# Kernel tuning notes

Hardware: AMD Instinct MI355X
Metric: run time of the kernel (lower is better)

The kernel has to match this reference:

```python
import jax, jax.numpy as jnp
import numpy as np

B, S, D = 4, 2048, 1024
E, ES, K = 16, 256, 4  # n_experts, expert_size, top-k (= n_heads)
STD_GATE = 0.02


def setup_inputs() -> dict:
    key = jax.random.key(0)
    k1, k2, k3, k4 = jax.random.split(key, 4)
    x = jax.random.normal(k1, (B, S, D), dtype=jnp.float32)
    # init per module: gate ~ N(0, d^-0.5), keys ~ N(0, d^-0.5), values ~ N(0, size^-0.5)
    w_gate = jax.random.normal(k2, (E, D), dtype=jnp.float32) * (D ** -0.5)
    keys = jax.random.normal(k3, (E, D, ES), dtype=jnp.float32) * (D ** -0.5)
    values = jax.random.normal(k4, (E, ES, D), dtype=jnp.float32) * ((E * ES) ** -0.5)
    return {"x": x, "w_gate": w_gate, "keys": keys, "values": values}


def reference(x, w_gate, keys, values):
    # sigma-MoE forward (selection_mode='sigmoid', activation=relu,
    # num_selected = n_heads = K, no bias, no dropout, eval mode)
    xt = x.reshape(-1, D)                         # [T, D]
    T = xt.shape[0]
    logits = xt @ w_gate.T                        # [T, E]
    sel = jax.nn.sigmoid(logits)                  # sigmoid gating
    sel_val, sel_idx = jax.lax.top_k(sel, K)      # [T, K]
    # sparse gate weights as dense [T, E] mask (zeros for unselected experts)
    gate_w = jnp.zeros((T, E), dtype=x.dtype).at[
        jnp.arange(T)[:, None], sel_idx
    ].set(sel_val)
    # per-expert hidden: h[t,e,s] = relu(sum_d x[t,d] keys[e,d,s])
    h = jax.nn.relu(jnp.einsum('td,eds->tes', xt, keys))  # [T, E, ES]
    # weighted scatter back through values: out = sum_e gate * h_e @ values_e
    out = jnp.einsum('tes,te,esv->tv', h, gate_w, values)  # [T, D]
    return out.reshape(B, S, D)
```

## Files before the change

kernel.cpp:

```cpp
#include <hip/hip_runtime.h>
#include <hip/hip_bf16.h>
#include <stdint.h>

#define T_TOK 8192
#define DIM   1024
#define NEXP  16
#define ESZ   256
#define TOPK  4
#define BM    64
#define BK    64
#define NPAIR (T_TOK*TOPK)
#define NGB   (T_TOK/32)
#define NBLK  128
#define GPB   (NGB/NBLK)
#define MAXROWS (NPAIR + NEXP*BM)
#define MAXTILES (NPAIR/BM + NEXP)

typedef __hip_bfloat16 bf16;
typedef short bf16x8 __attribute__((ext_vector_type(8)));
typedef float f32x4 __attribute__((ext_vector_type(4)));

__device__ __forceinline__ unsigned short f2bu(float f){
  __hip_bfloat16 b = __float2bfloat16(f);
  return *reinterpret_cast<unsigned short*>(&b);
}
__device__ __forceinline__ float bu2f(unsigned short u){
  __hip_bfloat16 b = *reinterpret_cast<__hip_bfloat16*>(&u);
  return __bfloat162float(b);
}

__device__ __forceinline__ void gload16(const void* g, void* l){
  __builtin_amdgcn_global_load_lds((const __attribute__((address_space(1))) void*)g,
                                   (__attribute__((address_space(3))) void*)l, 16, 0, 0);
}

__global__ __launch_bounds__(512) void k_gate(const float* __restrict__ x,
    const float* __restrict__ wg, bf16* __restrict__ xb,
    int* __restrict__ sel_idx, float* __restrict__ sel_gate,
    int* __restrict__ block_hist)
{
  __shared__ float wlds[NEXP*DIM];
  __shared__ int h[NEXP];
  const int tid = threadIdx.x;
  {
    const float4* src = (const float4*)wg;
    float4* dst = (float4*)wlds;
#pragma unroll
    for (int i=0;i<8;i++) dst[tid + i*512] = src[tid + i*512];
  }
  if (tid < NEXP) h[tid] = 0;
  __syncthreads();

  {
    const float* xs = x + (size_t)blockIdx.x*32*DIM;
    unsigned short* xd = (unsigned short*)xb + (size_t)blockIdx.x*32*DIM;
#pragma unroll
    for (int i=0;i<16;i++){
      const int f = tid + i*512;
      float4 v = *(const float4*)(xs + (size_t)f*4);
      ushort4 o; o.x=f2bu(v.x); o.y=f2bu(v.y); o.z=f2bu(v.z); o.w=f2bu(v.w);
      *(ushort4*)(xd + (size_t)f*4) = o;
    }
  }

  const int ts = tid >> 5;
  const int dc = tid & 31;
  const int t0 = blockIdx.x*32 + ts;
  const int t1 = t0 + 16;
  const float* xr0 = x + (size_t)t0*DIM;
  const float* xr1 = x + (size_t)t1*DIM;

  float acc0[NEXP], acc1[NEXP];
#pragma unroll
  for (int e=0;e<NEXP;e++){ acc0[e]=0.f; acc1[e]=0.f; }

#pragma unroll
  for (int i=0;i<8;i++){
    const int d0 = i*128 + dc*4;
    float4 xv0 = *(const float4*)(xr0 + d0);
    float4 xv1 = *(const float4*)(xr1 + d0);
#pragma unroll
    for (int e=0;e<NEXP;e++){
      float4 w = *(const float4*)(wlds + e*DIM + d0);
      acc0[e] += xv0.x*w.x + xv0.y*w.y + xv0.z*w.z + xv0.w*w.w;
      acc1[e] += xv1.x*w.x + xv1.y*w.y + xv1.z*w.z + xv1.w*w.w;
    }
  }

#pragma unroll
  for (int e=0;e<NEXP;e++){
#pragma unroll
    for (int s=1;s<32;s<<=1){
      acc0[e] += __shfl_xor(acc0[e], s);
      acc1[e] += __shfl_xor(acc1[e], s);
    }
  }

#pragma unroll
  for (int e=0;e<NEXP;e++){
    acc0[e] = 1.f/(1.f + expf(-acc0[e]));
    acc1[e] = 1.f/(1.f + expf(-acc1[e]));
  }
#pragma unroll
  for (int k=0;k<TOPK;k++){
    float b0=-2.f, b1=-2.f; int i0=0, i1=0;
#pragma unroll
    for (int e=0;e<NEXP;e++){
      if (acc0[e] > b0){ b0=acc0[e]; i0=e; }
      if (acc1[e] > b1){ b1=acc1[e]; i1=e; }
    }
    if (dc==0){
      sel_idx[t0*TOPK+k]=i0; sel_gate[t0*TOPK+k]=b0;
      sel_idx[t1*TOPK+k]=i1; sel_gate[t1*TOPK+k]=b1;
      atomicAdd(&h[i0],1); atomicAdd(&h[i1],1);
    }
    acc0[i0] = -2.f; acc1[i1] = -2.f;
  }
  __syncthreads();
  if (tid < NEXP) block_hist[blockIdx.x*NEXP + tid] = h[tid];
}

__global__ __launch_bounds__(256) void k_transpose2(const float* __restrict__ keys,
    const float* __restrict__ values, bf16* __restrict__ kT, bf16* __restrict__ vT)
{
  __shared__ float tile[32][33];
  const int which = blockIdx.y >> 4, e = blockIdx.y & 15;
  const int R = which ? ESZ : DIM, C = which ? DIM : ESZ;
  const float* src = (which ? values : keys) + (size_t)e*DIM*ESZ;
  bf16* dst = (which ? vT : kT) + (size_t)e*DIM*ESZ;
  const int ctiles = C/32;
  const int r0 = (blockIdx.x / ctiles)*32, c0 = (blockIdx.x % ctiles)*32;
  const int tx = threadIdx.x & 31, ty = threadIdx.x >> 5;
#pragma unroll
  for (int i=0;i<4;i++){ int r = ty + i*8; tile[r][tx] = src[(size_t)(r0+r)*C + c0 + tx]; }
  __syncthreads();
#pragma unroll
  for (int i=0;i<4;i++){ int r = ty + i*8; dst[(size_t)(c0+r)*R + r0 + tx] = __float2bfloat16(tile[tx][r]); }
}

__global__ void k_meta(const int* __restrict__ gh,
    int* __restrict__ tile_expert, int* __restrict__ tile_rowstart,
    int* __restrict__ tile_segend, int* __restrict__ block_base)
{
  __shared__ int sbc[NBLK][NEXP];
  __shared__ int cnt[NEXP], seg[NEXP];
  const int tid = threadIdx.x;
  for (int cell = tid; cell < NBLK*NEXP; cell += 256){
    int sb = cell >> 4, e = cell & 15;
    int s = 0;
#pragma unroll
    for (int g=0; g<GPB; ++g) s += gh[(sb*GPB+g)*NEXP + e];
    sbc[sb][e] = s;
  }
  __syncthreads();
  if (tid < NEXP){
    int s=0;
    for (int sb=0; sb<NBLK; sb++) s += sbc[sb][tid];
    cnt[tid]=s;
  }
  __syncthreads();
  if (tid==0){
    int off=0, tc=0;
    for (int e=0;e<NEXP;e++){
      seg[e]=off;
      int c = cnt[e];
      int nt = (c + BM - 1)/BM;
      for (int i=0;i<nt;i++){
        tile_expert[tc]=e; tile_rowstart[tc]=off+i*BM; tile_segend[tc]=off+c; tc++;
      }
      off += nt*BM;
    }
    for (; tc<MAXTILES; tc++) tile_expert[tc]=-1;
  }
  __syncthreads();
  if (tid < NEXP){
    int s = seg[tid];
    for (int sb=0; sb<NBLK; sb++){ block_base[sb*NEXP + tid] = s; s += sbc[sb][tid]; }
  }
}

__global__ __launch_bounds__(256) void k_scatter(const int* __restrict__ sel_idx,
    const float* __restrict__ sel_gate, const int* __restrict__ block_base,
    int* __restrict__ assign_token, float* __restrict__ assign_gate,
    int* __restrict__ inv_rows)
{
  __shared__ int wcnt[4][NEXP];
  const int p = blockIdx.x*256 + threadIdx.x;
  const int wave = threadIdx.x >> 6, lane = threadIdx.x & 63;
  const int e = sel_idx[p];
  const float g = sel_gate[p];
  int rank = 0;
#pragma unroll
  for (int ee=0; ee<NEXP; ee++){
    unsigned long long m = __ballot(e==ee);
    if (lane==0) wcnt[wave][ee] = (int)__popcll(m);
    if (e==ee) rank = (int)__popcll(m & ((1ull<<lane)-1ull));
  }
  __syncthreads();
  int pre = 0;
  for (int w=0; w<wave; w++) pre += wcnt[w][e];
  const int row = block_base[blockIdx.x*NEXP + e] + pre + rank;
  assign_token[row] = p >> 2;
  assign_gate[row]  = g;
  inv_rows[p] = row;
}

__global__ __launch_bounds__(256) void k_gemm1(
    const bf16* __restrict__ xb, const bf16* __restrict__ kT,
    const int* __restrict__ assign_token, const float* __restrict__ assign_gate,
    const int* __restrict__ tile_expert, const int* __restrict__ tile_rowstart,
    const int* __restrict__ tile_segend, bf16* __restrict__ h)
{
  __shared__ char smem[49152];
  __shared__ int   tokens_s[BM];
  __shared__ float gates_s[BM];

  const int nb = blockIdx.x, tile = blockIdx.y;
  const int e = tile_expert[tile];
  if (e < 0) return;
  const int row0 = tile_rowstart[tile];
  const int segend = tile_segend[tile];
  const int tid = threadIdx.x, wave = tid>>6, lane = tid&63;

  if (tid < BM){
    int rg = row0 + tid;
    bool vld = rg < segend;
    tokens_s[tid] = vld ? assign_token[rg] : 0;
    gates_s[tid]  = vld ? assign_gate[rg] : 0.f;
  }
  __syncthreads();

  const bf16* qA[2]; const bf16* qB[4]; int loA[2], loB[4];
#pragma unroll
  for (int i=0;i<2;i++){
    int row = i*32 + wave*8 + (lane>>3);
    int c   = (lane&7) ^ (row&7);
    qA[i] = xb + (size_t)tokens_s[row]*DIM + c*8;
    loA[i] = i*4096 + wave*1024;
  }
#pragma unroll
  for (int i=0;i<4;i++){
    int col = i*32 + wave*8 + (lane>>3);
    int c   = (lane&7) ^ (col&7);
    qB[i] = kT + ((size_t)e*ESZ + nb*128 + col)*DIM + c*8;
    loB[i] = i*4096 + wave*1024;
  }

  const int wr0 = (wave>>1)*32, wc0 = (wave&1)*64;
  int offA[2][2], offB[2][4];
#pragma unroll
  for (int kk=0;kk<2;kk++){
    int kb = kk*64 + (lane>>4)*16;
#pragma unroll
    for (int m=0;m<2;m++){ int row = wr0 + m*16 + (lane&15); offA[kk][m] = row*128 + (kb ^ ((row&7)<<4)); }
#pragma unroll
    for (int n=0;n<4;n++){ int col = wc0 + n*16 + (lane&15); offB[kk][n] = col*128 + (kb ^ ((col&7)<<4)); }
  }

  f32x4 acc[2][4];
#pragma unroll
  for (int m=0;m<2;m++)
#pragma unroll
    for (int n=0;n<4;n++) acc[m][n] = {0.f,0.f,0.f,0.f};

  auto stage = [&](int abase, int bbase){
#pragma unroll
    for (int i=0;i<2;i++){ gload16(qA[i], smem + abase + loA[i]); qA[i]+=BK; }
#pragma unroll
    for (int i=0;i<4;i++){ gload16(qB[i], smem + bbase + loB[i]); qB[i]+=BK; }
  };
  auto compute = [&](const char* Ab, const char* Bb){
#pragma unroll
    for (int kk=0;kk<2;kk++){
      bf16x8 af[2], bfr[4];
#pragma unroll
      for (int m=0;m<2;m++) af[m]  = *(const bf16x8*)(Ab + offA[kk][m]);
#pragma unroll
      for (int n=0;n<4;n++) bfr[n] = *(const bf16x8*)(Bb + offB[kk][n]);
#pragma unroll
      for (int m=0;m<2;m++)
#pragma unroll
        for (int n=0;n<4;n++)
          acc[m][n] = __builtin_amdgcn_mfma_f32_16x16x32_bf16(af[m], bfr[n], acc[m][n], 0,0,0);
    }
  };

  stage(0, 16384);
  asm volatile("s_waitcnt vmcnt(0)" ::: "memory");
  __builtin_amdgcn_s_barrier();

  for (int kt=0; kt<16; kt+=2){
    stage(8192, 32768);
    compute(smem, smem+16384);
    asm volatile("s_waitcnt vmcnt(0)" ::: "memory");
    __builtin_amdgcn_s_barrier();
    if (kt+2 < 16) stage(0, 16384);
    compute(smem+8192, smem+32768);
    asm volatile("s_waitcnt vmcnt(0)" ::: "memory");
    __builtin_amdgcn_s_barrier();
  }

#pragma unroll
  for (int m=0;m<2;m++)
#pragma unroll
    for (int n=0;n<4;n++){
      int col = wc0 + n*16 + (lane&15);
#pragma unroll
      for (int j=0;j<4;j++){
        int rloc = wr0 + m*16 + ((lane>>4)<<2) + j;
        float v = fmaxf(acc[m][n][j], 0.f) * gates_s[rloc];
        h[(size_t)(row0 + rloc)*ESZ + nb*128 + col] = __float2bfloat16(v);
      }
    }
}

__global__ __launch_bounds__(256) void k_gemm2(
    const bf16* __restrict__ h, const bf16* __restrict__ vT,
    const int* __restrict__ tile_expert, const int* __restrict__ tile_rowstart,
    bf16* __restrict__ partial)
{
  __shared__ char smem[49152];

  const int nb = blockIdx.x, tile = blockIdx.y;
  const int e = tile_expert[tile];
  if (e < 0) return;
  const int row0 = tile_rowstart[tile];
  const int tid = threadIdx.x, wave = tid>>6, lane = tid&63;

  const bf16* qA[2]; const bf16* qB[4]; int loA[2], loB[4];
#pragma unroll
  for (int i=0;i<2;i++){
    int row = i*32 + wave*8 + (lane>>3);
    int c   = (lane&7) ^ (row&7);
    qA[i] = h + (size_t)(row0 + row)*ESZ + c*8;
    loA[i] = i*4096 + wave*1024;
  }
#pragma unroll
  for (int i=0;i<4;i++){
    int col = i*32 + wave*8 + (lane>>3);
    int c   = (lane&7) ^ (col&7);
    qB[i] = vT + ((size_t)e*DIM + nb*128 + col)*ESZ + c*8;
    loB[i] = i*4096 + wave*1024;
  }

  const int wr0 = (wave>>1)*32, wc0 = (wave&1)*64;
  int offA[2][2], offB[2][4];
#pragma unroll
  for (int kk=0;kk<2;kk++){
    int kb = kk*64 + (lane>>4)*16;
#pragma unroll
    for (int m=0;m<2;m++){ int row = wr0 + m*16 + (lane&15); offA[kk][m] = row*128 + (kb ^ ((row&7)<<4)); }
#pragma unroll
    for (int n=0;n<4;n++){ int col = wc0 + n*16 + (lane&15); offB[kk][n] = col*128 + (kb ^ ((col&7)<<4)); }
  }

  f32x4 acc[2][4];
#pragma unroll
  for (int m=0;m<2;m++)
#pragma unroll
    for (int n=0;n<4;n++) acc[m][n] = {0.f,0.f,0.f,0.f};

  auto stage = [&](int abase, int bbase){
#pragma unroll
    for (int i=0;i<2;i++){ gload16(qA[i], smem + abase + loA[i]); qA[i]+=BK; }
#pragma unroll
    for (int i=0;i<4;i++){ gload16(qB[i], smem + bbase + loB[i]); qB[i]+=BK; }
  };
  auto compute = [&](const char* Ab, const char* Bb){
#pragma unroll
    for (int kk=0;kk<2;kk++){
      bf16x8 af[2], bfr[4];
#pragma unroll
      for (int m=0;m<2;m++) af[m]  = *(const bf16x8*)(Ab + offA[kk][m]);
#pragma unroll
      for (int n=0;n<4;n++) bfr[n] = *(const bf16x8*)(Bb + offB[kk][n]);
#pragma unroll
      for (int m=0;m<2;m++)
#pragma unroll
        for (int n=0;n<4;n++)
          acc[m][n] = __builtin_amdgcn_mfma_f32_16x16x32_bf16(af[m], bfr[n], acc[m][n], 0,0,0);
    }
  };

  stage(0, 16384);
  asm volatile("s_waitcnt vmcnt(0)" ::: "memory");
  __builtin_amdgcn_s_barrier();

  stage(8192, 32768);
  compute(smem, smem+16384);
  asm volatile("s_waitcnt vmcnt(0)" ::: "memory");
  __builtin_amdgcn_s_barrier();
  stage(0, 16384);
  compute(smem+8192, smem+32768);
  asm volatile("s_waitcnt vmcnt(0)" ::: "memory");
  __builtin_amdgcn_s_barrier();
  stage(8192, 32768);
  compute(smem, smem+16384);
  asm volatile("s_waitcnt vmcnt(0)" ::: "memory");
  __builtin_amdgcn_s_barrier();
  compute(smem+8192, smem+32768);

#pragma unroll
  for (int m=0;m<2;m++)
#pragma unroll
    for (int n=0;n<4;n++){
      int col = wc0 + n*16 + (lane&15);
#pragma unroll
      for (int j=0;j<4;j++){
        int rloc = wr0 + m*16 + ((lane>>4)<<2) + j;
        partial[(size_t)(row0 + rloc)*DIM + nb*128 + col] = __float2bfloat16(acc[m][n][j]);
      }
    }
}

__global__ __launch_bounds__(256) void k_reduce(const bf16* __restrict__ partial,
    const int* __restrict__ inv_rows, float* __restrict__ out)
{
  const int t = blockIdx.x;
  const int c0 = threadIdx.x * 4;
  int rows[TOPK];
#pragma unroll
  for (int k=0;k<TOPK;k++) rows[k] = inv_rows[t*TOPK+k];
  float a0=0.f,a1=0.f,a2=0.f,a3=0.f;
#pragma unroll
  for (int k=0;k<TOPK;k++){
    ushort4 v = *(const ushort4*)((const unsigned short*)partial + (size_t)rows[k]*DIM + c0);
    a0 += bu2f(v.x); a1 += bu2f(v.y); a2 += bu2f(v.z); a3 += bu2f(v.w);
  }
  float4 o = {a0,a1,a2,a3};
  *(float4*)(out + (size_t)t*DIM + c0) = o;
}

extern "C" void kernel_launch(void* const* d_in, const int* in_sizes, int n_in,
                              void* d_out, int out_size, void* d_ws, size_t ws_size,
                              hipStream_t stream)
{
  const float* x      = (const float*)d_in[0];
  const float* wg     = (const float*)d_in[1];
  const float* keys   = (const float*)d_in[2];
  const float* values = (const float*)d_in[3];
  float* out = (float*)d_out;

  char* ws = (char*)d_ws;
  size_t off = 0;
  bf16* vT   = (bf16*)(ws+off); off += (size_t)NEXP*DIM*ESZ*2;
  bf16* hbuf = (bf16*)(ws+off); off += (size_t)MAXROWS*ESZ*2;
  int*   sel_idx      = (int*)  (ws+off); off += (size_t)NPAIR*4;
  float* sel_gate     = (float*)(ws+off); off += (size_t)NPAIR*4;
  int*   assign_token = (int*)  (ws+off); off += (size_t)MAXROWS*4;
  float* assign_gate  = (float*)(ws+off); off += (size_t)MAXROWS*4;
  int*   inv_rows     = (int*)  (ws+off); off += (size_t)NPAIR*4;
  int*   block_hist   = (int*)  (ws+off); off += (size_t)NGB*NEXP*4;
  int*   block_base   = (int*)  (ws+off); off += (size_t)NBLK*NEXP*4;
  int*   tile_expert  = (int*)  (ws+off); off += 4096;
  int*   tile_rowstart= (int*)  (ws+off); off += 4096;
  int*   tile_segend  = (int*)  (ws+off); off += 4096;
  const size_t PARTIAL_BYTES = (size_t)MAXROWS*DIM*2;
  const size_t XB_BYTES = (size_t)T_TOK*DIM*2;
  const size_t KT_BYTES = (size_t)NEXP*ESZ*DIM*2;
  bf16* partial = (bf16*)(ws+off); off += PARTIAL_BYTES;
  bf16* xb = (bf16*)((char*)partial + PARTIAL_BYTES - XB_BYTES - KT_BYTES);
  bf16* kT = (bf16*)((char*)partial + PARTIAL_BYTES - KT_BYTES);

  k_gate<<<NGB, 512, 0, stream>>>(x, wg, xb, sel_idx, sel_gate, block_hist);
  k_transpose2<<<dim3(256, NEXP*2), 256, 0, stream>>>(keys, values, kT, vT);
  k_meta<<<1, 256, 0, stream>>>(block_hist, tile_expert, tile_rowstart, tile_segend, block_base);
  k_scatter<<<NBLK, 256, 0, stream>>>(sel_idx, sel_gate, block_base, assign_token,
      assign_gate, inv_rows);
  k_gemm1<<<dim3(2, MAXTILES), 256, 0, stream>>>(xb, kT, assign_token, assign_gate,
      tile_expert, tile_rowstart, tile_segend, hbuf);
  k_gemm2<<<dim3(8, MAXTILES), 256, 0, stream>>>(hbuf, vT,
      tile_expert, tile_rowstart, partial);
  k_reduce<<<T_TOK, 256, 0, stream>>>(partial, inv_rows, out);
}
```

Baseline: 152.3 us.

## Split gate kernel into half-dim dot kernel and separate top-4 kernel

The gating kernel is split in two. The first kernel runs 1024 blocks, each computing partial logits over half of D for 16 tokens, fusing the bf16 conversion of x into the same loads and writing the partials to a workspace buffer. The second kernel sums the two halves, applies the sigmoid, does top-4 selection with one thread per token, and writes 64-token histograms that match k_meta's 128 sub-blocks, which simplifies k_meta. This aims for more parallelism and a smaller LDS footprint per block, at the cost of an extra launch and a round trip for the partial logits.

```diff
diff --git a/kernel.cpp b/kernel.cpp
--- a/kernel.cpp
+++ b/kernel.cpp
@@ -10,9 +10,7 @@
 #define BM    64
 #define BK    64
 #define NPAIR (T_TOK*TOPK)
-#define NGB   (T_TOK/32)
 #define NBLK  128
-#define GPB   (NGB/NBLK)
 #define MAXROWS (NPAIR + NEXP*BM)
 #define MAXTILES (NPAIR/BM + NEXP)
 
@@ -34,54 +32,50 @@
                                    (__attribute__((address_space(3))) void*)l, 16, 0, 0);
 }
 
-__global__ __launch_bounds__(512) void k_gate(const float* __restrict__ x,
-    const float* __restrict__ wg, bf16* __restrict__ xb,
-    int* __restrict__ sel_idx, float* __restrict__ sel_gate,
-    int* __restrict__ block_hist)
-{
-  __shared__ float wlds[NEXP*DIM];
-  __shared__ int h[NEXP];
+__global__ __launch_bounds__(256) void k_gate_dot(const float* __restrict__ x,
+    const float* __restrict__ wg, bf16* __restrict__ xb, float* __restrict__ plog)
+{
+  __shared__ float wlds[NEXP*512];
   const int tid = threadIdx.x;
+  const int half = blockIdx.x & 1;
+  const int tg   = blockIdx.x >> 1;
+
   {
     const float4* src = (const float4*)wg;
     float4* dst = (float4*)wlds;
 #pragma unroll
-    for (int i=0;i<8;i++) dst[tid + i*512] = src[tid + i*512];
-  }
-  if (tid < NEXP) h[tid] = 0;
-  __syncthreads();
-
-  {
-    const float* xs = x + (size_t)blockIdx.x*32*DIM;
-    unsigned short* xd = (unsigned short*)xb + (size_t)blockIdx.x*32*DIM;
-#pragma unroll
-    for (int i=0;i<16;i++){
-      const int f = tid + i*512;
-      float4 v = *(const float4*)(xs + (size_t)f*4);
-      ushort4 o; o.x=f2bu(v.x); o.y=f2bu(v.y); o.z=f2bu(v.z); o.w=f2bu(v.w);
-      *(ushort4*)(xd + (size_t)f*4) = o;
-    }
-  }
+    for (int i=0;i<8;i++){
+      int idx = tid + i*256;
+      int e = idx >> 7, d4 = idx & 127;
+      dst[idx] = src[e*256 + half*128 + d4];
+    }
+  }
+  __syncthreads();
 
   const int ts = tid >> 5;
   const int dc = tid & 31;
-  const int t0 = blockIdx.x*32 + ts;
-  const int t1 = t0 + 16;
-  const float* xr0 = x + (size_t)t0*DIM;
-  const float* xr1 = x + (size_t)t1*DIM;
+  const int t0 = tg*16 + ts, t1 = t0 + 8;
+  const float* xr0 = x + (size_t)t0*DIM + half*512;
+  const float* xr1 = x + (size_t)t1*DIM + half*512;
+  unsigned short* xd0 = (unsigned short*)xb + (size_t)t0*DIM + half*512;
+  unsigned short* xd1 = (unsigned short*)xb + (size_t)t1*DIM + half*512;
 
   float acc0[NEXP], acc1[NEXP];
 #pragma unroll
   for (int e=0;e<NEXP;e++){ acc0[e]=0.f; acc1[e]=0.f; }
 
 #pragma unroll
-  for (int i=0;i<8;i++){
+  for (int i=0;i<4;i++){
     const int d0 = i*128 + dc*4;
     float4 xv0 = *(const float4*)(xr0 + d0);
     float4 xv1 = *(const float4*)(xr1 + d0);
+    ushort4 o0; o0.x=f2bu(xv0.x); o0.y=f2bu(xv0.y); o0.z=f2bu(xv0.z); o0.w=f2bu(xv0.w);
+    ushort4 o1; o1.x=f2bu(xv1.x); o1.y=f2bu(xv1.y); o1.z=f2bu(xv1.z); o1.w=f2bu(xv1.w);
+    *(ushort4*)(xd0 + d0) = o0;
+    *(ushort4*)(xd1 + d0) = o1;
 #pragma unroll
     for (int e=0;e<NEXP;e++){
-      float4 w = *(const float4*)(wlds + e*DIM + d0);
+      float4 w = *(const float4*)(wlds + e*512 + d0);
       acc0[e] += xv0.x*w.x + xv0.y*w.y + xv0.z*w.z + xv0.w*w.w;
       acc1[e] += xv1.x*w.x + xv1.y*w.y + xv1.z*w.z + xv1.w*w.w;
     }
@@ -96,28 +90,50 @@
     }
   }
 
-#pragma unroll
-  for (int e=0;e<NEXP;e++){
-    acc0[e] = 1.f/(1.f + expf(-acc0[e]));
-    acc1[e] = 1.f/(1.f + expf(-acc1[e]));
+  if (dc==0){
+    float* p0 = plog + (size_t)t0*32 + half*16;
+    float* p1 = plog + (size_t)t1*32 + half*16;
+#pragma unroll
+    for (int i=0;i<4;i++){
+      f32x4 v0 = {acc0[i*4],acc0[i*4+1],acc0[i*4+2],acc0[i*4+3]};
+      f32x4 v1 = {acc1[i*4],acc1[i*4+1],acc1[i*4+2],acc1[i*4+3]};
+      *(f32x4*)(p0 + i*4) = v0;
+      *(f32x4*)(p1 + i*4) = v1;
+    }
+  }
+}
+
+__global__ __launch_bounds__(256) void k_gate_top4(const float* __restrict__ plog,
+    int* __restrict__ sel_idx, float* __restrict__ sel_gate,
+    int* __restrict__ block_hist)
+{
+  __shared__ int h[4][NEXP];
+  const int tid = threadIdx.x;
+  if (tid < 64) h[tid>>4][tid&15] = 0;
+  __syncthreads();
+
+  const int t = blockIdx.x*256 + tid;
+  const float* p = plog + (size_t)t*32;
+  float v[NEXP];
+#pragma unroll
+  for (int i=0;i<4;i++){
+    f32x4 a = *(const f32x4*)(p + i*4);
+    f32x4 b = *(const f32x4*)(p + 16 + i*4);
+#pragma unroll
+    for (int j=0;j<4;j++) v[i*4+j] = 1.f/(1.f + expf(-(a[j]+b[j])));
   }
 #pragma unroll
   for (int k=0;k<TOPK;k++){
-    float b0=-2.f, b1=-2.f; int i0=0, i1=0;
-#pragma unroll
-    for (int e=0;e<NEXP;e++){
-      if (acc0[e] > b0){ b0=acc0[e]; i0=e; }
-      if (acc1[e] > b1){ b1=acc1[e]; i1=e; }
-    }
-    if (dc==0){
-      sel_idx[t0*TOPK+k]=i0; sel_gate[t0*TOPK+k]=b0;
-      sel_idx[t1*TOPK+k]=i1; sel_gate[t1*TOPK+k]=b1;
-      atomicAdd(&h[i0],1); atomicAdd(&h[i1],1);
-    }
-    acc0[i0] = -2.f; acc1[i1] = -2.f;
-  }
-  __syncthreads();
-  if (tid < NEXP) block_hist[blockIdx.x*NEXP + tid] = h[tid];
+    float bv=-2.f; int bi=0;
+#pragma unroll
+    for (int e=0;e<NEXP;e++) if (v[e] > bv){ bv=v[e]; bi=e; }
+    sel_idx[t*TOPK+k]=bi; sel_gate[t*TOPK+k]=bv;
+    atomicAdd(&h[tid>>6][bi],1);
+    v[bi] = -2.f;
+  }
+  __syncthreads();
+  if (tid < 64)
+    block_hist[((size_t)blockIdx.x*4 + (tid>>4))*NEXP + (tid&15)] = h[tid>>4][tid&15];
 }
 
 __global__ __launch_bounds__(256) void k_transpose2(const float* __restrict__ keys,
@@ -145,13 +161,8 @@
   __shared__ int sbc[NBLK][NEXP];
   __shared__ int cnt[NEXP], seg[NEXP];
   const int tid = threadIdx.x;
-  for (int cell = tid; cell < NBLK*NEXP; cell += 256){
-    int sb = cell >> 4, e = cell & 15;
-    int s = 0;
-#pragma unroll
-    for (int g=0; g<GPB; ++g) s += gh[(sb*GPB+g)*NEXP + e];
-    sbc[sb][e] = s;
-  }
+  for (int cell = tid; cell < NBLK*NEXP; cell += 256)
+    sbc[cell>>4][cell&15] = gh[cell];
   __syncthreads();
   if (tid < NEXP){
     int s=0;
@@ -445,12 +456,13 @@
   size_t off = 0;
   bf16* vT   = (bf16*)(ws+off); off += (size_t)NEXP*DIM*ESZ*2;
   bf16* hbuf = (bf16*)(ws+off); off += (size_t)MAXROWS*ESZ*2;
+  float* plog         = (float*)(ws+off); off += (size_t)T_TOK*32*4;
   int*   sel_idx      = (int*)  (ws+off); off += (size_t)NPAIR*4;
   float* sel_gate     = (float*)(ws+off); off += (size_t)NPAIR*4;
   int*   assign_token = (int*)  (ws+off); off += (size_t)MAXROWS*4;
   float* assign_gate  = (float*)(ws+off); off += (size_t)MAXROWS*4;
   int*   inv_rows     = (int*)  (ws+off); off += (size_t)NPAIR*4;
-  int*   block_hist   = (int*)  (ws+off); off += (size_t)NGB*NEXP*4;
+  int*   block_hist   = (int*)  (ws+off); off += (size_t)NBLK*NEXP*4;
   int*   block_base   = (int*)  (ws+off); off += (size_t)NBLK*NEXP*4;
   int*   tile_expert  = (int*)  (ws+off); off += 4096;
   int*   tile_rowstart= (int*)  (ws+off); off += 4096;
@@ -462,7 +474,8 @@
   bf16* xb = (bf16*)((char*)partial + PARTIAL_BYTES - XB_BYTES - KT_BYTES);
   bf16* kT = (bf16*)((char*)partial + PARTIAL_BYTES - KT_BYTES);
 
-  k_gate<<<NGB, 512, 0, stream>>>(x, wg, xb, sel_idx, sel_gate, block_hist);
+  k_gate_dot<<<T_TOK/16*2, 256, 0, stream>>>(x, wg, xb, plog);
+  k_gate_top4<<<T_TOK/256, 256, 0, stream>>>(plog, sel_idx, sel_gate, block_hist);
   k_transpose2<<<dim3(256, NEXP*2), 256, 0, stream>>>(keys, values, kT, vT);
   k_meta<<<1, 256, 0, stream>>>(block_hist, tile_expert, tile_rowstart, tile_segend, block_base);
   k_scatter<<<NBLK, 256, 0, stream>>>(sel_idx, sel_gate, block_base, assign_token,
```

New measurement: 145.4 us. 1.05x faster.
